# Optimization experiments

Measured on AMD Instinct MI355X. Metric: run time of the kernel, lower is better.

## Reference

```python
import jax, jax.numpy as jnp
import numpy as np

jax.config.update("jax_enable_x64", True)

NNZ = 8_388_608        # number of sparse (feature_id, value) pairs
N_FEATURES = 8_192     # number of calibrated feature ids
N_BIN = 63             # bin boundaries per feature -> 64 bins
OUT_BITS = 22          # output id space = 1 << 22
GOLDEN32 = np.uint32(0x9E3779B9)  # Knuth multiplicative-hashing constant


def setup_inputs() -> dict:
    key = jax.random.key(0)
    k1, k2, k3 = jax.random.split(key, 3)
    input_keys = jax.random.randint(k1, (NNZ,), 0, 2 * N_FEATURES, dtype=jnp.int64)
    input_vals = jax.random.normal(k2, (NNZ,), dtype=jnp.float32)
    # Calibrated feature ids (sorted) and per-feature sorted bin boundaries.
    feature_ids = jnp.arange(N_FEATURES, dtype=jnp.int64)
    bin_vals = jnp.sort(
        jax.random.normal(k3, (N_FEATURES, N_BIN), dtype=jnp.float32), axis=1
    ).reshape(-1)
    return {
        "input_keys": input_keys,
        "input_vals": input_vals,
        "feature_ids": feature_ids,
        "bin_vals": bin_vals,
    }


def _lower_bound_bins(bin_vals_flat, feat_idx, vals, n_bin):
    """Per-value branchless binary search: bin = sum(bin_row < val).

    bin_vals_flat: [F * n_bin] row-sorted boundaries, feat_idx: [nnz] int,
    vals: [nnz] float. Returns [nnz] int32 bin index in [0, n_bin].
    """
    steps = int(np.ceil(np.log2(n_bin + 1)))  # 6 for n_bin=63
    base = feat_idx.astype(jnp.int64) * n_bin
    lo = jnp.zeros(vals.shape, dtype=jnp.int32)
    hi = jnp.full(vals.shape, n_bin, dtype=jnp.int32)
    for _ in range(steps):
        mid = (lo + hi) >> 1                       # in [0, n_bin]
        mid_safe = jnp.minimum(mid, n_bin - 1)     # gather-safe
        bv = bin_vals_flat[base + mid_safe]
        valid = lo < hi
        go_right = valid & (bv < vals)             # strict '<' => lower bound
        lo = jnp.where(go_right, mid + 1, lo)
        hi = jnp.where(valid & ~go_right, mid, hi)
    return lo


def reference(input_keys, input_vals, feature_ids, bin_vals):
    F = feature_ids.shape[0]
    n_bin = bin_vals.shape[0] // F
    mask = jnp.int64((1 << OUT_BITS) - 1)

    # --- find each key in the (sorted) calibrated feature-id table ---
    idx = jnp.searchsorted(feature_ids, input_keys)          # [nnz]
    idx_safe = jnp.minimum(idx, F - 1)
    calibrated = feature_ids[idx_safe] == input_keys          # [nnz] bool

    # --- bin assignment: bin = sum(bin_vals_row < val) ---
    bins = _lower_bound_bins(bin_vals, idx_safe, input_vals, n_bin)

    # --- 32-bit integer multiplicative hash of (feature_id, bin) ---
    h = (input_keys.astype(jnp.uint32) * GOLDEN32 + bins.astype(jnp.uint32)) * GOLDEN32
    hashed_key = h.astype(jnp.int64) & mask

    out_keys = jnp.where(calibrated, hashed_key, input_keys & mask)
    out_vals = jnp.where(calibrated, jnp.ones_like(input_vals), input_vals)
    # dense_shape of the resulting SparseTensor is [batch, 1 << OUT_BITS]
    return out_keys, out_vals
```

## Files before the change

kernel.cpp:

```cpp
#include <hip/hip_runtime.h>
#include <stdint.h>
#include <math.h>


#define GOLDEN   0x9E3779B9u
#define OUT_MASK ((1u << 22) - 1u)
#define NBIN  63
#define QROWF 80
#define NKEY  16384
#define NPIV  8192
#define MASKW (NKEY / 32)

typedef float fx4 __attribute__((ext_vector_type(4)));
typedef int   ix4 __attribute__((ext_vector_type(4)));

__global__ __launch_bounds__(256) void build_tables_kernel(
    const int* __restrict__ fids, const float* __restrict__ bins,
    float* __restrict__ qtab, uint4* __restrict__ gpiv,
    unsigned* __restrict__ gmask, int F)
{
    const int t = blockIdx.x * blockDim.x + threadIdx.x;
    if (t >= F * QROWF) return;
    const int r = t / QROWF;
    const int j = t - r * QROWF;
    const int q = j / 20;
    const int u = j - q * 20;
    const float* src = bins + (size_t)r * NBIN;

    int bi;
    if (u < 3)       bi = 16 * q + 4 * u + 3;
    else if (u == 3) bi = -1;
    else             bi = 16 * q + (u - 4);
    float val = (bi >= 0 && bi < NBIN) ? src[bi] : INFINITY;
    if (u == 3) val = 0.0f;
    qtab[t] = val;

    if (j == 0) {
        const int k = fids[r];
        if ((unsigned)k < (unsigned)NKEY) {
            atomicOr(&gmask[k >> 5], 1u << (k & 31));
            if ((unsigned)k < (unsigned)NPIV) {
                uint4 p;
                p.x = __float_as_uint(src[15]);
                p.y = __float_as_uint(src[31]);
                p.z = __float_as_uint(src[47]);
                p.w = (unsigned)r;
                gpiv[k] = p;
            }
        }
    }
}

__device__ __forceinline__ void hd_fallback(
    int k, float v, const int* __restrict__ fids, const float* __restrict__ bins,
    int F, int fsteps, float& okey, float& oval)
{
    int lo = 0, hi = F;
    for (int s = 0; s < fsteps; ++s) {
        int  mid  = (lo + hi) >> 1;
        int  mids = min(mid, F - 1);
        int  fv   = fids[mids];
        bool valid = lo < hi;
        bool right = valid && (fv < k);
        lo = right ? mid + 1 : lo;
        hi = (valid && !right) ? mid : hi;
    }
    const int  idx_safe   = min(lo, F - 1);
    const bool calibrated = (fids[idx_safe] == k);
    const float* brow = bins + (size_t)idx_safe * NBIN;
    int blo = 0, bhi = NBIN;
    #pragma unroll
    for (int s = 0; s < 6; ++s) {
        int   mid  = (blo + bhi) >> 1;
        int   mids = min(mid, NBIN - 1);
        float bv   = brow[mids];
        bool  valid = blo < bhi;
        bool  right = valid && (bv < v);
        blo = right ? mid + 1 : blo;
        bhi = (valid && !right) ? mid : bhi;
    }
    const uint32_t h = ((uint32_t)k * GOLDEN + (uint32_t)blo) * GOLDEN;
    okey = calibrated ? (float)(h & OUT_MASK) : (float)((uint32_t)k & OUT_MASK);
    oval = calibrated ? 1.0f : v;
}

__global__ __launch_bounds__(1024) void hd_main_kernel(
    const int* __restrict__ keys, const float* __restrict__ vals,
    const int* __restrict__ fids, const float* __restrict__ bins,
    const float* __restrict__ qtab, const uint4* __restrict__ gpiv,
    const unsigned* __restrict__ gmask,
    float* __restrict__ out_keys, float* __restrict__ out_vals,
    int n, int F, int fsteps)
{
    extern __shared__ char smem[];
    uint4*    spiv  = reinterpret_cast<uint4*>(smem);
    unsigned* smask = reinterpret_cast<unsigned*>(smem + (size_t)NPIV * sizeof(uint4));

    const int tid = threadIdx.x;
    for (int i = tid; i < NPIV; i += (int)blockDim.x) spiv[i] = gpiv[i];
    if (tid < MASKW) smask[tid] = gmask[tid];
    __syncthreads();

    const int gid = blockIdx.x * blockDim.x + tid;
    const int i0 = gid * 8;
    if (i0 >= n) return;

    int   ks[8];
    float vs[8];
    const bool full = (i0 + 7 < n);
    if (full) {
        const ix4 ka = __builtin_nontemporal_load(reinterpret_cast<const ix4*>(keys + i0));
        const ix4 kb = __builtin_nontemporal_load(reinterpret_cast<const ix4*>(keys + i0 + 4));
        const fx4 va = __builtin_nontemporal_load(reinterpret_cast<const fx4*>(vals + i0));
        const fx4 vb = __builtin_nontemporal_load(reinterpret_cast<const fx4*>(vals + i0 + 4));
        ks[0]=ka.x; ks[1]=ka.y; ks[2]=ka.z; ks[3]=ka.w;
        ks[4]=kb.x; ks[5]=kb.y; ks[6]=kb.z; ks[7]=kb.w;
        vs[0]=va.x; vs[1]=va.y; vs[2]=va.z; vs[3]=va.w;
        vs[4]=vb.x; vs[5]=vb.y; vs[6]=vb.z; vs[7]=vb.w;
    } else {
        #pragma unroll
        for (int j = 0; j < 8; ++j) {
            int idx = min(i0 + j, n - 1);
            ks[j] = keys[idx];
            vs[j] = vals[idx];
        }
    }

    float ok[8], ov[8];
    #pragma unroll
    for (int j = 0; j < 8; ++j) {
        const int   k = ks[j];
        const float v = vs[j];
        if ((unsigned)k < (unsigned)NKEY) {
            const bool calib = (smask[(unsigned)k >> 5] >> (k & 31)) & 1u;
            if (calib) {
                if ((unsigned)k < (unsigned)NPIV) {
                    const uint4 p = spiv[k];
                    const float p0 = __uint_as_float(p.x);
                    const float p1 = __uint_as_float(p.y);
                    const float p2 = __uint_as_float(p.z);
                    const int q = (p0 < v) + (p1 < v) + (p2 < v);
                    const float* qbase = qtab + (size_t)p.w * QROWF + q * 20;
                    const fx4 qh = *reinterpret_cast<const fx4*>(qbase);
                    const int s = (qh.x < v) + (qh.y < v) + (qh.z < v);
                    const fx4 leaf = *reinterpret_cast<const fx4*>(qbase + 4 + 4 * s);
                    const int cnt = 16 * q + 4 * s
                        + (leaf.x < v) + (leaf.y < v) + (leaf.z < v) + (leaf.w < v);
                    const uint32_t h = ((uint32_t)k * GOLDEN + (uint32_t)cnt) * GOLDEN;
                    ok[j] = (float)(h & OUT_MASK);
                    ov[j] = 1.0f;
                } else {
                    hd_fallback(k, v, fids, bins, F, fsteps, ok[j], ov[j]);
                }
            } else {
                ok[j] = (float)((uint32_t)k & OUT_MASK);
                ov[j] = v;
            }
        } else {
            hd_fallback(k, v, fids, bins, F, fsteps, ok[j], ov[j]);
        }
    }

    if (full) {
        fx4 a, b;
        a.x=ok[0]; a.y=ok[1]; a.z=ok[2]; a.w=ok[3];
        b.x=ok[4]; b.y=ok[5]; b.z=ok[6]; b.w=ok[7];
        __builtin_nontemporal_store(a, reinterpret_cast<fx4*>(out_keys + i0));
        __builtin_nontemporal_store(b, reinterpret_cast<fx4*>(out_keys + i0 + 4));
        a.x=ov[0]; a.y=ov[1]; a.z=ov[2]; a.w=ov[3];
        b.x=ov[4]; b.y=ov[5]; b.z=ov[6]; b.w=ov[7];
        __builtin_nontemporal_store(a, reinterpret_cast<fx4*>(out_vals + i0));
        __builtin_nontemporal_store(b, reinterpret_cast<fx4*>(out_vals + i0 + 4));
    } else {
        for (int j = 0; j < 8 && i0 + j < n; ++j) {
            out_keys[i0 + j] = ok[j];
            out_vals[i0 + j] = ov[j];
        }
    }
}

__global__ __launch_bounds__(256) void hd_simple_kernel(
    const int* __restrict__ keys, const float* __restrict__ vals,
    const int* __restrict__ fids, const float* __restrict__ bins,
    float* __restrict__ out_keys, float* __restrict__ out_vals,
    int n, int F, int fsteps)
{
    const int gid = blockIdx.x * blockDim.x + threadIdx.x;
    const int i0 = gid * 4;
    if (i0 >= n) return;
    #pragma unroll
    for (int j = 0; j < 4; ++j) {
        int idx = min(i0 + j, n - 1);
        float okey, oval;
        hd_fallback(keys[idx], vals[idx], fids, bins, F, fsteps, okey, oval);
        if (i0 + j < n) { out_keys[i0 + j] = okey; out_vals[i0 + j] = oval; }
    }
}

extern "C" void kernel_launch(void* const* d_in, const int* in_sizes, int n_in,
                              void* d_out, int out_size, void* d_ws, size_t ws_size,
                              hipStream_t stream) {
    const int*   keys = (const int*)d_in[0];
    const float* vals = (const float*)d_in[1];
    const int*   fids = (const int*)d_in[2];
    const float* bins = (const float*)d_in[3];

    const int n = in_sizes[0];
    const int F = in_sizes[2];

    int fsteps = 0;
    while ((1 << fsteps) < F + 1) ++fsteps;

    float* out_keys = (float*)d_out;
    float* out_vals = (float*)d_out + n;

    const size_t qtab_bytes = (size_t)F * QROWF * sizeof(float);
    const size_t ws_need    = qtab_bytes + (size_t)NPIV * 16 + (size_t)MASKW * 4;
    const size_t lds_bytes  = (size_t)NPIV * 16 + (size_t)MASKW * 4;

    int max_lds = 0;
    hipDeviceGetAttribute(&max_lds, hipDeviceAttributeMaxSharedMemoryPerBlock, 0);

    const bool fast = (ws_size >= ws_need) && ((size_t)max_lds >= lds_bytes) &&
                      (in_sizes[3] == F * NBIN);

    if (fast) {
        float*    qtab  = (float*)d_ws;
        uint4*    gpiv  = (uint4*)((char*)d_ws + qtab_bytes);
        unsigned* gmask = (unsigned*)((char*)gpiv + (size_t)NPIV * 16);

        hipMemsetAsync(gmask, 0, (size_t)MASKW * 4, stream);
        build_tables_kernel<<<(F * QROWF + 255) / 256, 256, 0, stream>>>(
            fids, bins, qtab, gpiv, gmask, F);

        (void)hipFuncSetAttribute(
            reinterpret_cast<const void*>(hd_main_kernel),
            hipFuncAttributeMaxDynamicSharedMemorySize, (int)lds_bytes);

        const int threads = 1024;
        const int grid = (n + threads * 8 - 1) / (threads * 8);
        hd_main_kernel<<<grid, threads, lds_bytes, stream>>>(
            keys, vals, fids, bins, qtab, gpiv, gmask,
            out_keys, out_vals, n, F, fsteps);
    } else {
        const int threads = 256;
        const int grid = (n + threads * 4 - 1) / (threads * 4);
        hd_simple_kernel<<<grid, threads, 0, stream>>>(
            keys, vals, fids, bins, out_keys, out_vals, n, F, fsteps);
    }
}
```

Before: 177.8 us.

## Replace 3-level quaternary bin search with 3-way pivot plus linear section scan

Bin tables are rebuilt as three 21-entry sections (padded to 24 floats) indexed directly by key, with two pivot floats per key in LDS instead of a uint4 holding three pivots and a row index. The lookup does one LDS pivot compare, then loads six contiguous float4s and counts them, replacing two dependent global loads with one independent batch. This shortens the dependent memory-latency chain and halves LDS per block, at the cost of more bytes fetched and more compares per element. Table rows are now indexed by key rather than row, which assumes unique fids below NPIV.

```diff
diff --git a/kernel.cpp b/kernel.cpp
--- a/kernel.cpp
+++ b/kernel.cpp
@@ -6,48 +6,42 @@
 #define GOLDEN   0x9E3779B9u
 #define OUT_MASK ((1u << 22) - 1u)
 #define NBIN  63
-#define QROWF 80
+#define SECL  21
+#define SECP  24
+#define QROWF 72
 #define NKEY  16384
 #define NPIV  8192
 #define MASKW (NKEY / 32)
 
 typedef float fx4 __attribute__((ext_vector_type(4)));
 typedef int   ix4 __attribute__((ext_vector_type(4)));
+typedef float fx2 __attribute__((ext_vector_type(2)));
 
 __global__ __launch_bounds__(256) void build_tables_kernel(
     const int* __restrict__ fids, const float* __restrict__ bins,
-    float* __restrict__ qtab, uint4* __restrict__ gpiv,
+    float* __restrict__ qtab, fx2* __restrict__ gpiv,
     unsigned* __restrict__ gmask, int F)
 {
     const int t = blockIdx.x * blockDim.x + threadIdx.x;
     if (t >= F * QROWF) return;
     const int r = t / QROWF;
     const int j = t - r * QROWF;
-    const int q = j / 20;
-    const int u = j - q * 20;
+    const int k = fids[r];
+
+    if (j == 0 && (unsigned)k < (unsigned)NKEY) {
+        atomicOr(&gmask[k >> 5], 1u << (k & 31));
+    }
+    if ((unsigned)k >= (unsigned)NPIV) return;
+
     const float* src = bins + (size_t)r * NBIN;
-
-    int bi;
-    if (u < 3)       bi = 16 * q + 4 * u + 3;
-    else if (u == 3) bi = -1;
-    else             bi = 16 * q + (u - 4);
-    float val = (bi >= 0 && bi < NBIN) ? src[bi] : INFINITY;
-    if (u == 3) val = 0.0f;
-    qtab[t] = val;
+    const int q = j / SECP;
+    const int u = j - q * SECP;
+    const int bi = SECL * q + u;
+    qtab[(size_t)k * QROWF + j] = (u < SECL && bi < NBIN) ? src[bi] : INFINITY;
 
     if (j == 0) {
-        const int k = fids[r];
-        if ((unsigned)k < (unsigned)NKEY) {
-            atomicOr(&gmask[k >> 5], 1u << (k & 31));
-            if ((unsigned)k < (unsigned)NPIV) {
-                uint4 p;
-                p.x = __float_as_uint(src[15]);
-                p.y = __float_as_uint(src[31]);
-                p.z = __float_as_uint(src[47]);
-                p.w = (unsigned)r;
-                gpiv[k] = p;
-            }
-        }
+        fx2 p; p.x = src[20]; p.y = src[41];
+        gpiv[k] = p;
     }
 }
 
@@ -87,14 +81,14 @@
 __global__ __launch_bounds__(1024) void hd_main_kernel(
     const int* __restrict__ keys, const float* __restrict__ vals,
     const int* __restrict__ fids, const float* __restrict__ bins,
-    const float* __restrict__ qtab, const uint4* __restrict__ gpiv,
+    const float* __restrict__ qtab, const fx2* __restrict__ gpiv,
     const unsigned* __restrict__ gmask,
     float* __restrict__ out_keys, float* __restrict__ out_vals,
     int n, int F, int fsteps)
 {
     extern __shared__ char smem[];
-    uint4*    spiv  = reinterpret_cast<uint4*>(smem);
-    unsigned* smask = reinterpret_cast<unsigned*>(smem + (size_t)NPIV * sizeof(uint4));
+    fx2*      spiv  = reinterpret_cast<fx2*>(smem);
+    unsigned* smask = reinterpret_cast<unsigned*>(smem + (size_t)NPIV * sizeof(fx2));
 
     const int tid = threadIdx.x;
     for (int i = tid; i < NPIV; i += (int)blockDim.x) spiv[i] = gpiv[i];
@@ -135,17 +129,19 @@
             const bool calib = (smask[(unsigned)k >> 5] >> (k & 31)) & 1u;
             if (calib) {
                 if ((unsigned)k < (unsigned)NPIV) {
-                    const uint4 p = spiv[k];
-                    const float p0 = __uint_as_float(p.x);
-                    const float p1 = __uint_as_float(p.y);
-                    const float p2 = __uint_as_float(p.z);
-                    const int q = (p0 < v) + (p1 < v) + (p2 < v);
-                    const float* qbase = qtab + (size_t)p.w * QROWF + q * 20;
-                    const fx4 qh = *reinterpret_cast<const fx4*>(qbase);
-                    const int s = (qh.x < v) + (qh.y < v) + (qh.z < v);
-                    const fx4 leaf = *reinterpret_cast<const fx4*>(qbase + 4 + 4 * s);
-                    const int cnt = 16 * q + 4 * s
-                        + (leaf.x < v) + (leaf.y < v) + (leaf.z < v) + (leaf.w < v);
+                    const fx2 p = spiv[k];
+                    const int t = (p.x < v) + (p.y < v);
+                    const fx4* sec = reinterpret_cast<const fx4*>(
+                        qtab + (size_t)(unsigned)k * QROWF + t * SECP);
+                    const fx4 b0 = sec[0], b1 = sec[1], b2 = sec[2],
+                              b3 = sec[3], b4 = sec[4], b5 = sec[5];
+                    const int cnt = SECL * t
+                        + (b0.x < v) + (b0.y < v) + (b0.z < v) + (b0.w < v)
+                        + (b1.x < v) + (b1.y < v) + (b1.z < v) + (b1.w < v)
+                        + (b2.x < v) + (b2.y < v) + (b2.z < v) + (b2.w < v)
+                        + (b3.x < v) + (b3.y < v) + (b3.z < v) + (b3.w < v)
+                        + (b4.x < v) + (b4.y < v) + (b4.z < v) + (b4.w < v)
+                        + (b5.x < v) + (b5.y < v) + (b5.z < v) + (b5.w < v);
                     const uint32_t h = ((uint32_t)k * GOLDEN + (uint32_t)cnt) * GOLDEN;
                     ok[j] = (float)(h & OUT_MASK);
                     ov[j] = 1.0f;
@@ -214,9 +210,10 @@
     float* out_keys = (float*)d_out;
     float* out_vals = (float*)d_out + n;
 
-    const size_t qtab_bytes = (size_t)F * QROWF * sizeof(float);
-    const size_t ws_need    = qtab_bytes + (size_t)NPIV * 16 + (size_t)MASKW * 4;
-    const size_t lds_bytes  = (size_t)NPIV * 16 + (size_t)MASKW * 4;
+    const size_t qtab_bytes = (size_t)NPIV * QROWF * sizeof(float);
+    const size_t gpiv_bytes = (size_t)NPIV * sizeof(fx2);
+    const size_t ws_need    = qtab_bytes + gpiv_bytes + (size_t)MASKW * 4;
+    const size_t lds_bytes  = gpiv_bytes + (size_t)MASKW * 4;
 
     int max_lds = 0;
     hipDeviceGetAttribute(&max_lds, hipDeviceAttributeMaxSharedMemoryPerBlock, 0);
@@ -226,8 +223,8 @@
 
     if (fast) {
         float*    qtab  = (float*)d_ws;
-        uint4*    gpiv  = (uint4*)((char*)d_ws + qtab_bytes);
-        unsigned* gmask = (unsigned*)((char*)gpiv + (size_t)NPIV * 16);
+        fx2*      gpiv  = (fx2*)((char*)d_ws + qtab_bytes);
+        unsigned* gmask = (unsigned*)((char*)gpiv + gpiv_bytes);
 
         hipMemsetAsync(gmask, 0, (size_t)MASKW * 4, stream);
         build_tables_kernel<<<(F * QROWF + 255) / 256, 256, 0, stream>>>(
```

Measured after the change: 177.7 us. Within noise of the previous version (-0.0%).
